# Kernel tuning notes

Hardware: AMD Instinct MI355X
Metric: run time of the kernel (lower is better)

The kernel has to match this reference:

```python
import jax, jax.numpy as jnp
import numpy as np

DN = ('NCHW', 'OIHW', 'NCHW')

def conv3x3(x, w):
    # stride-1, SAME padding, no bias (matches build_conv_layer(..., 3, stride=1, padding='same', bias=False))
    return jax.lax.conv_general_dilated(x, w, window_strides=(1, 1), padding='SAME', dimension_numbers=DN)

def setup_inputs() -> dict:
    key = jax.random.key(0)
    k1, k2, k3, k4 = jax.random.split(key, 4)
    B, C, H, W = 4, 256, 64, 64
    inputs = jax.random.normal(k1, (B, C, H, W), dtype=jnp.float32)
    ref = jax.random.normal(k2, (B, C, H, W), dtype=jnp.float32)
    # xavier-uniform-ish conv weights, [O, I, kH, kW]
    fan = C * 9
    lim = np.sqrt(6.0 / (fan + fan)).astype(np.float32)
    w1 = jax.random.uniform(k3, (C, C, 3, 3), dtype=jnp.float32, minval=-lim, maxval=lim)
    w2 = jax.random.uniform(k4, (C, C, 3, 3), dtype=jnp.float32, minval=-lim, maxval=lim)
    gamma = jnp.float32(0.5)
    return {'inputs': inputs, 'ref': ref, 'w1': w1, 'w2': w2, 'gamma': gamma}

def reference(inputs, ref, w1, w2, gamma):
    # Faithful to source: x0 = relu(conv1(inputs)) is computed then immediately
    # overwritten by a view of x1 (a bug in the original), so inputs only
    # contributes its shape. We execute the dead conv for FLOP parity.
    _dead = jax.nn.relu(conv3x3(inputs, w1))
    x1 = jax.nn.relu(conv3x3(ref, w1))            # [B, C, H, W]
    B, C, H, W = x1.shape
    q = x1.transpose(0, 2, 3, 1).reshape(B, H * W, C)   # [B, HW, C]
    k = x1.reshape(B, C, H * W)                          # [B, C, HW]
    scores = jnp.einsum('bnc,bcm->bnm', q, k)            # [B, HW, HW]
    corr = jax.nn.softmax(scores, axis=1)                # softmax over dim=1 (atypical axis)
    v = jax.nn.relu(conv3x3(ref, w2)).reshape(B, C, H * W)  # [B, C, HW]
    A = jnp.einsum('bcn,bnm->bcm', v, corr).reshape(inputs.shape)
    return A * gamma + ref
```

## Files before the change

kernel.cpp:

```cpp
#include <hip/hip_runtime.h>
#include <math.h>

#define CDIM 256
#define NSEQ 4096
#define HWDIM 64
#define PPIX 4356

typedef unsigned short u16;
typedef __attribute__((ext_vector_type(8))) short bf16x8;
typedef __attribute__((ext_vector_type(4))) float f32x4;
typedef __attribute__((ext_vector_type(16))) float f32x16;

__device__ __forceinline__ u16 f2bf(float f) {
    unsigned u = __float_as_uint(f);
    unsigned r = (u + 0x7FFFu + ((u >> 16) & 1u)) >> 16;
    return (u16)r;
}

__device__ __forceinline__ void gload_lds16(const u16* g, u16* l) {
    __builtin_amdgcn_global_load_lds(
        (const __attribute__((address_space(1))) unsigned int*)g,
        (__attribute__((address_space(3))) unsigned int*)l, 16, 0, 0);
}

__global__ __launch_bounds__(256)
void pad_transpose_kernel(const float* __restrict__ x, u16* __restrict__ padded)
{
    __shared__ float lds[64 * 65];
    const int tid = threadIdx.x;
    const int y = blockIdx.x, c0 = blockIdx.y << 6, b = blockIdx.z;
    #pragma unroll
    for (int i = 0; i < 16; ++i) {
        int f = tid + (i << 8);
        int c = f >> 6, xx = f & 63;
        lds[c * 65 + xx] = x[(((size_t)(b * CDIM + c0 + c)) * HWDIM + y) * HWDIM + xx];
    }
    __syncthreads();
    #pragma unroll
    for (int i = 0; i < 2; ++i) {
        int f = tid + (i << 8);
        int xx = f >> 3, c8 = f & 7;
        union { u16 h[8]; float4 v; } pk;
        #pragma unroll
        for (int j = 0; j < 8; ++j) pk.h[j] = f2bf(lds[(c8 * 8 + j) * 65 + xx]);
        *(float4*)&padded[((size_t)b * PPIX + (y + 1) * 66 + (xx + 1)) * CDIM + c0 + (c8 << 3)] = pk.v;
    }
}

__global__ __launch_bounds__(256)
void w_prepack_kernel(const float* __restrict__ w, u16* __restrict__ wk)
{
    int t = (blockIdx.x << 8) + threadIdx.x;
    const float* wp = w + (size_t)t * 9;
    #pragma unroll
    for (int j = 0; j < 9; ++j) wk[j * 65536 + t] = f2bf(wp[j]);
}

__device__ __forceinline__ void conv_stage(const u16* __restrict__ padded,
                                           const u16* __restrict__ wk,
                                           u16* Xb, u16* Wb,
                                           int b, int y0, int cb, int t,
                                           int wv, int lane)
{
    const int kyx = t >> 2, cib = (t & 3) << 6;
    const int ky = kyx / 3, kx = kyx - ky * 3;
    #pragma unroll
    for (int i = 0; i < 2; ++i) {
        int f = ((i << 2) + wv) << 6;
        int fl = f + lane;
        int r = fl >> 3;
        int gsw = (fl & 7) ^ (r & 7);
        gload_lds16(&padded[((size_t)b * PPIX + (y0 + ky) * 66 + r + kx) * CDIM + cib + (gsw << 3)],
                    Xb + (f << 3));
    }
    #pragma unroll
    for (int i = 0; i < 4; ++i) {
        int f = ((i << 2) + wv) << 6;
        int fl = f + lane;
        int r = fl >> 3;
        int gsw = (fl & 7) ^ (r & 7);
        gload_lds16(&wk[((size_t)kyx << 16) + (size_t)(cb + r) * 256 + cib + (gsw << 3)],
                    Wb + (f << 3));
    }
}

template <bool OA>
__global__ __launch_bounds__(256)
void conv_mfma_kernel(const u16* __restrict__ padded, const u16* __restrict__ wk,
                      u16* __restrict__ out)
{
    __shared__ alignas(16) u16 smem[24576];

    const int tid = threadIdx.x;
    const int lane = tid & 63, wv = tid >> 6;
    const int lr = lane & 15, lg = lane >> 4;
    const int cb = blockIdx.x << 7;
    const int y0 = blockIdx.y;
    const int b = blockIdx.z;

    constexpr int MF = OA ? 4 : 2;
    constexpr int NF = OA ? 2 : 4;
    f32x4 acc[MF][NF] = {};

    conv_stage(padded, wk, smem, smem + 8192, b, y0, cb, 0, wv, lane);
    __syncthreads();

    int cur = 0;
    for (int t = 0; t < 36; ++t) {
        if (t + 1 < 36)
            conv_stage(padded, wk, smem + (cur ^ 1) * 4096,
                       smem + 8192 + (cur ^ 1) * 8192, b, y0, cb, t + 1, wv, lane);

        const u16* Xs = smem + cur * 4096;
        const u16* Ws = smem + 8192 + cur * 8192;

        #pragma unroll
        for (int kk = 0; kk < 2; ++kk) {
            const int ca = ((kk << 5) + (lg << 3)) ^ ((lr & 7) << 3);
            if constexpr (OA) {
                bf16x8 a[4], bb[2];
                #pragma unroll
                for (int mf = 0; mf < 4; ++mf)
                    a[mf] = *(const bf16x8*)&Xs[((mf * 16 + lr) << 6) + ca];
                #pragma unroll
                for (int nf = 0; nf < 2; ++nf)
                    bb[nf] = *(const bf16x8*)&Ws[((wv * 32 + nf * 16 + lr) << 6) + ca];
                #pragma unroll
                for (int mf = 0; mf < 4; ++mf)
                    #pragma unroll
                    for (int nf = 0; nf < 2; ++nf)
                        acc[mf][nf] = __builtin_amdgcn_mfma_f32_16x16x32_bf16(a[mf], bb[nf], acc[mf][nf], 0, 0, 0);
            } else {
                bf16x8 a[2], bb[4];
                #pragma unroll
                for (int mf = 0; mf < 2; ++mf)
                    a[mf] = *(const bf16x8*)&Ws[((wv * 32 + mf * 16 + lr) << 6) + ca];
                #pragma unroll
                for (int nf = 0; nf < 4; ++nf)
                    bb[nf] = *(const bf16x8*)&Xs[((nf * 16 + lr) << 6) + ca];
                #pragma unroll
                for (int mf = 0; mf < 2; ++mf)
                    #pragma unroll
                    for (int nf = 0; nf < 4; ++nf)
                        acc[mf][nf] = __builtin_amdgcn_mfma_f32_16x16x32_bf16(a[mf], bb[nf], acc[mf][nf], 0, 0, 0);
            }
        }
        __syncthreads();
        cur ^= 1;
    }

    const int m0 = y0 << 6;
    if constexpr (OA) {
        #pragma unroll
        for (int mf = 0; mf < 4; ++mf)
            #pragma unroll
            for (int nf = 0; nf < 2; ++nf) {
                int nb = m0 + mf * 16 + lg * 4;
                int co = cb + wv * 32 + nf * 16 + lr;
                union { u16 h[4]; uint2 v; } pk;
                #pragma unroll
                for (int j = 0; j < 4; ++j) pk.h[j] = f2bf(fmaxf(acc[mf][nf][j], 0.f));
                *(uint2*)&out[((size_t)(b * CDIM + co)) * NSEQ + nb] = pk.v;
            }
    } else {
        #pragma unroll
        for (int mf = 0; mf < 2; ++mf)
            #pragma unroll
            for (int nf = 0; nf < 4; ++nf) {
                int cob = cb + wv * 32 + mf * 16 + lg * 4;
                int n = m0 + nf * 16 + lr;
                union { u16 h[4]; uint2 v; } pk;
                #pragma unroll
                for (int j = 0; j < 4; ++j) pk.h[j] = f2bf(fmaxf(acc[mf][nf][j], 0.f));
                *(uint2*)&out[((size_t)(b * NSEQ + n)) * CDIM + cob] = pk.v;
            }
    }
}

__global__ __launch_bounds__(256)
void rownorm_kernel(const u16* __restrict__ XT, float* __restrict__ rn2,
                    float* __restrict__ bmax)
{
    __shared__ float wmax[4];
    const int tid = threadIdx.x;
    const int lane = tid & 63, wv = tid >> 6;
    const int row = (blockIdx.x << 2) + wv;
    const u16* xp = &XT[(size_t)row * CDIM + (lane << 2)];
    uint2 v = *(const uint2*)xp;
    float s = 0.f;
    #pragma unroll
    for (int j = 0; j < 4; ++j) {
        unsigned hu = (j & 1) ? ((&v.x)[j >> 1] >> 16) : ((&v.x)[j >> 1] & 0xFFFFu);
        float x = __uint_as_float(hu << 16);
        s += x * x;
    }
    #pragma unroll
    for (int off = 1; off < 64; off <<= 1) s += __shfl_xor(s, off);
    if (lane == 0) {
        rn2[row] = s;
        wmax[wv] = s;
    }
    __syncthreads();
    if (tid == 0)
        bmax[blockIdx.x] = fmaxf(fmaxf(wmax[0], wmax[1]), fmaxf(wmax[2], wmax[3]));
}

__global__ __launch_bounds__(256)
void maxred_kernel(const float* __restrict__ bmax, float* __restrict__ maxrn2)
{
    __shared__ float wred[4];
    const int tid = threadIdx.x;
    const int lane = tid & 63, wv = tid >> 6;
    const int b = blockIdx.x;
    float m = 0.f;
    #pragma unroll
    for (int i = 0; i < 4; ++i)
        m = fmaxf(m, bmax[(b << 10) + (i << 8) + tid]);
    #pragma unroll
    for (int off = 1; off < 64; off <<= 1) m = fmaxf(m, __shfl_xor(m, off));
    if (lane == 0) wred[wv] = m;
    __syncthreads();
    if (tid == 0)
        maxrn2[b] = fmaxf(fmaxf(wred[0], wred[1]), fmaxf(wred[2], wred[3]));
}

#define M_TILE 128
#define NC 64
#define NCHUNKS 32

#define KS_OFF 0
#define VS_OFF 32768
#define P_OFF  65536

__device__ __forceinline__ void stage_chunk(const u16* __restrict__ XT, const u16* __restrict__ Vn,
                                            u16* Kb, u16* Vb, int b, int n0, int wv, int lane)
{
    #pragma unroll
    for (int i = 0; i < 4; ++i) {
        int f = ((i << 3) + wv) << 6;
        int fl = f + lane;
        int r = fl >> 5;
        int gsw = (fl & 31) ^ (r & 15);
        gload_lds16(&XT[(size_t)(b * NSEQ + n0 + r) * CDIM + (gsw << 3)], Kb + (f << 3));
    }
    #pragma unroll
    for (int i = 0; i < 4; ++i) {
        int f = ((i << 3) + wv) << 6;
        int fl = f + lane;
        int r = fl >> 3;
        int gsw = (fl & 7) ^ (r & 7);
        gload_lds16(&Vn[(size_t)(b * CDIM + r) * NSEQ + n0 + (gsw << 3)], Vb + (f << 3));
    }
}

__global__ __launch_bounds__(512, 2)
void attn_part_kernel(const u16* __restrict__ XT, const u16* __restrict__ Vn,
                      const float* __restrict__ rn2, const float* __restrict__ maxrn2,
                      float* __restrict__ o0, u16* __restrict__ o1,
                      float* __restrict__ lsum)
{
    __shared__ alignas(16) u16 smem[73728];
    u16* Ps = smem + P_OFF;

    const int tid = threadIdx.x;
    const int lane = tid & 63;
    const int wv = tid >> 6;
    const int l31 = lane & 31;
    const int hi = lane >> 5;
    const int bh = blockIdx.x;
    const int b = bh >> 1, h = bh & 1;
    const int m0 = blockIdx.y * M_TILE;
    const int nbase = h * (NSEQ / 2);

    const int qt = wv & 3;
    const int kh = wv >> 2;
    const int qa = qt * 32 + l31;
    const int qsel = wv & 1;
    const int csel = wv >> 1;

    const float mq = sqrtf(rn2[(size_t)b * NSEQ + m0 + qa]) * sqrtf(maxrn2[b]);

    bf16x8 qreg[16];
    {
        const u16* qrow = &XT[(size_t)(b * NSEQ + m0 + qa) * CDIM + (hi << 3)];
        #pragma unroll
        for (int ks = 0; ks < 16; ++ks)
            qreg[ks] = *(const bf16x8*)(qrow + (ks << 4));
    }

    f32x16 o[2][2] = {};
    float lrun = 0.f;

    stage_chunk(XT, Vn, smem + KS_OFF, smem + VS_OFF, b, nbase, wv, lane);
    __syncthreads();

    int cur = 0;
    for (int ci = 0; ci < NCHUNKS; ++ci) {
        if (ci + 1 < NCHUNKS)
            stage_chunk(XT, Vn, smem + KS_OFF + (cur ^ 1) * 16384,
                        smem + VS_OFF + (cur ^ 1) * 16384,
                        b, nbase + (ci + 1) * NC, wv, lane);

        const u16* Kc = smem + KS_OFF + cur * 16384;
        const u16* Vc = smem + VS_OFF + cur * 16384;

        f32x16 s0 = {}, s1 = {};
        {
            const int krow = kh * 32 + l31;
            const u16* kbase = &Kc[krow << 8];
            const int ksw = krow & 15;
            __builtin_amdgcn_s_setprio(1);
            #pragma unroll
            for (int ks = 0; ks < 16; ks += 2) {
                bf16x8 ka0 = *(const bf16x8*)&kbase[((((ks + 0) << 1) + hi) ^ ksw) << 3];
                bf16x8 ka1 = *(const bf16x8*)&kbase[((((ks + 1) << 1) + hi) ^ ksw) << 3];
                s0 = __builtin_amdgcn_mfma_f32_32x32x16_bf16(ka0, qreg[ks], s0, 0, 0, 0);
                s1 = __builtin_amdgcn_mfma_f32_32x32x16_bf16(ka1, qreg[ks + 1], s1, 0, 0, 0);
            }
            __builtin_amdgcn_s_setprio(0);
        }
        f32x16 s = s0 + s1;

        float p[16];
        float ps = 0.f;
        #pragma unroll
        for (int r = 0; r < 16; ++r) { p[r] = __expf(s[r] - mq); ps += p[r]; }
        ps += __shfl_xor(ps, 32);
        lrun += ps;

        {
            const int swz = qa & 7;
            #pragma unroll
            for (int r4 = 0; r4 < 4; ++r4) {
                union { u16 h4[4]; uint2 v; } pk;
                pk.h4[0] = f2bf(p[r4 * 4 + 0]); pk.h4[1] = f2bf(p[r4 * 4 + 1]);
                pk.h4[2] = f2bf(p[r4 * 4 + 2]); pk.h4[3] = f2bf(p[r4 * 4 + 3]);
                int g = (kh << 2) + r4;
                *(uint2*)&Ps[(qa << 6) + (((g ^ swz) << 3) | (hi << 2))] = pk.v;
            }
        }
        __syncthreads();

        {
            const int q0 = ((qsel << 1) + 0) * 32 + l31;
            const int q1 = ((qsel << 1) + 1) * 32 + l31;
            const int c0 = ((csel << 1) + 0) * 32 + l31;
            const int c1 = ((csel << 1) + 1) * 32 + l31;
            __builtin_amdgcn_s_setprio(1);
            #pragma unroll
            for (int ks = 0; ks < 4; ++ks) {
                const int gp = (ks << 1) + hi;
                bf16x8 pb0 = *(const bf16x8*)&Ps[(q0 << 6) + ((gp ^ (q0 & 7)) << 3)];
                bf16x8 pb1 = *(const bf16x8*)&Ps[(q1 << 6) + ((gp ^ (q1 & 7)) << 3)];
                bf16x8 va0 = *(const bf16x8*)&Vc[(c0 << 6) + ((gp ^ (c0 & 7)) << 3)];
                bf16x8 va1 = *(const bf16x8*)&Vc[(c1 << 6) + ((gp ^ (c1 & 7)) << 3)];
                o[0][0] = __builtin_amdgcn_mfma_f32_32x32x16_bf16(va0, pb0, o[0][0], 0, 0, 0);
                o[0][1] = __builtin_amdgcn_mfma_f32_32x32x16_bf16(va1, pb0, o[0][1], 0, 0, 0);
                o[1][0] = __builtin_amdgcn_mfma_f32_32x32x16_bf16(va0, pb1, o[1][0], 0, 0, 0);
                o[1][1] = __builtin_amdgcn_mfma_f32_32x32x16_bf16(va1, pb1, o[1][1], 0, 0, 0);
            }
            __builtin_amdgcn_s_setprio(0);
        }

        __syncthreads();
        cur ^= 1;
    }

    if (lane < 32)
        lsum[(size_t)(((h * 2 + kh) * 4 + b)) * NSEQ + m0 + qa] = lrun;

    #pragma unroll
    for (int qi = 0; qi < 2; ++qi) {
        const int q = m0 + ((qsel << 1) + qi) * 32 + l31;
        #pragma unroll
        for (int cj = 0; cj < 2; ++cj) {
            #pragma unroll
            for (int reg = 0; reg < 16; ++reg) {
                int c = ((csel << 1) + cj) * 32 + (reg & 3) + ((reg >> 2) << 3) + (hi << 2);
                size_t oi = ((size_t)(b * CDIM + c)) * NSEQ + q;
                if (h == 0) o0[oi] = o[qi][cj][reg];
                else        o1[oi] = f2bf(o[qi][cj][reg]);
            }
        }
    }
}

__global__ __launch_bounds__(256)
void merge_kernel(float* __restrict__ out, const u16* __restrict__ o1,
                  const float* __restrict__ lsum, const float* __restrict__ ref,
                  const float* __restrict__ gptr)
{
    const int f = (blockIdx.x << 8) + threadIdx.x;
    const int n4 = f & 1023;
    const int c = (f >> 10) & 255;
    const int b = f >> 18;
    const float g = gptr[0];

    float4 p0 = ((const float4*)out)[f];
    uint2 q1 = *(const uint2*)&o1[((size_t)(b * CDIM + c)) * NSEQ + (n4 << 2)];
    float4 rf = ((const float4*)ref)[f];

    float res[4];
    #pragma unroll
    for (int j = 0; j < 4; ++j) {
        int row = (n4 << 2) + j;
        float l = lsum[(size_t)(0 * 4 + b) * NSEQ + row]
                + lsum[(size_t)(1 * 4 + b) * NSEQ + row]
                + lsum[(size_t)(2 * 4 + b) * NSEQ + row]
                + lsum[(size_t)(3 * 4 + b) * NSEQ + row];
        float rl = 1.0f / l;
        float v0 = ((const float*)&p0)[j];
        unsigned hu = ((j & 1) ? ((&q1.x)[j >> 1] >> 16) : ((&q1.x)[j >> 1] & 0xFFFFu));
        float v1 = __uint_as_float(hu << 16);
        float a = (v0 + v1) * rl;
        res[j] = g * a + ((const float*)&rf)[j];
    }
    ((float4*)out)[f] = *(float4*)res;
}

extern "C" void kernel_launch(void* const* d_in, const int* in_sizes, int n_in,
                              void* d_out, int out_size, void* d_ws, size_t ws_size,
                              hipStream_t stream)
{
    const float* ref = (const float*)d_in[1];
    const float* w1  = (const float*)d_in[2];
    const float* w2  = (const float*)d_in[3];
    const float* gma = (const float*)d_in[4];
    float* out = (float*)d_out;

    u16* XT     = (u16*)d_ws;
    u16* Vn     = XT + (size_t)4 * NSEQ * CDIM;
    u16* padded = Vn + (size_t)4 * NSEQ * CDIM;
    u16* wk1    = padded + (size_t)4 * PPIX * CDIM;
    u16* wk2    = wk1 + (size_t)9 * 65536;
    u16*   o1     = padded;
    float* lsum   = (float*)wk1;
    float* rn2    = (float*)wk2;
    float* bmax   = rn2 + 16384;
    float* maxrn2 = bmax + 4096;

    hipMemsetAsync(padded, 0, (size_t)4 * PPIX * CDIM * sizeof(u16), stream);
    pad_transpose_kernel<<<dim3(64, 4, 4), 256, 0, stream>>>(ref, padded);
    w_prepack_kernel<<<dim3(256), 256, 0, stream>>>(w1, wk1);
    w_prepack_kernel<<<dim3(256), 256, 0, stream>>>(w2, wk2);

    dim3 cgrid(2, 64, 4);
    conv_mfma_kernel<false><<<cgrid, 256, 0, stream>>>(padded, wk1, XT);
    conv_mfma_kernel<true ><<<cgrid, 256, 0, stream>>>(padded, wk2, Vn);

    rownorm_kernel<<<dim3(4096), 256, 0, stream>>>(XT, rn2, bmax);
    maxred_kernel<<<dim3(4), 256, 0, stream>>>(bmax, maxrn2);

    attn_part_kernel<<<dim3(8, NSEQ / M_TILE), 512, 0, stream>>>(XT, Vn, rn2, maxrn2, out, o1, lsum);
    merge_kernel<<<dim3((4 * CDIM * NSEQ / 4) / 256), 256, 0, stream>>>(out, o1, lsum, ref, gma);
}
```

Before: 168.8 us.

## Use 16-wave blocks with 128-key chunks and single-buffered LDS in attention

The attention kernel now runs 1024 threads (16 waves) per block and stages 128 keys per chunk instead of 64, halving the chunk count. The double-buffered K/V staging is replaced by a single buffer with an explicit vmcnt wait and barrier. Each wave now owns one 32-channel slice of the PV product, and the softmax row sums are split into 8 partials that the merge kernel adds up. The goal is fewer barriers per key and more waves to hide latency. The risks are that load/compute overlap is lost without double buffering, and the larger block caps registers per thread, which could cause spills given the 64 registers held for Q.

```diff
diff --git a/kernel.cpp b/kernel.cpp
--- a/kernel.cpp
+++ b/kernel.cpp
@@ -225,19 +225,20 @@
 }
 
 #define M_TILE 128
-#define NC 64
-#define NCHUNKS 32
-
-#define KS_OFF 0
+#define NC 128
+#define NCHUNKS 16
+
 #define VS_OFF 32768
 #define P_OFF  65536
 
-__device__ __forceinline__ void stage_chunk(const u16* __restrict__ XT, const u16* __restrict__ Vn,
-                                            u16* Kb, u16* Vb, int b, int n0, int wv, int lane)
+__device__ __forceinline__ void stage_chunk128(const u16* __restrict__ XT,
+                                               const u16* __restrict__ Vn,
+                                               u16* Kb, u16* Vb,
+                                               int b, int n0, int wid, int lane)
 {
     #pragma unroll
     for (int i = 0; i < 4; ++i) {
-        int f = ((i << 3) + wv) << 6;
+        int f = ((i << 4) + wid) << 6;
         int fl = f + lane;
         int r = fl >> 5;
         int gsw = (fl & 31) ^ (r & 15);
@@ -245,26 +246,26 @@
     }
     #pragma unroll
     for (int i = 0; i < 4; ++i) {
-        int f = ((i << 3) + wv) << 6;
+        int f = ((i << 4) + wid) << 6;
         int fl = f + lane;
-        int r = fl >> 3;
-        int gsw = (fl & 7) ^ (r & 7);
+        int r = fl >> 4;
+        int gsw = (fl & 15) ^ (r & 7);
         gload_lds16(&Vn[(size_t)(b * CDIM + r) * NSEQ + n0 + (gsw << 3)], Vb + (f << 3));
     }
 }
 
-__global__ __launch_bounds__(512, 2)
+__global__ __launch_bounds__(1024, 4)
 void attn_part_kernel(const u16* __restrict__ XT, const u16* __restrict__ Vn,
                       const float* __restrict__ rn2, const float* __restrict__ maxrn2,
                       float* __restrict__ o0, u16* __restrict__ o1,
                       float* __restrict__ lsum)
 {
-    __shared__ alignas(16) u16 smem[73728];
+    __shared__ alignas(16) u16 smem[81920];
     u16* Ps = smem + P_OFF;
 
     const int tid = threadIdx.x;
     const int lane = tid & 63;
-    const int wv = tid >> 6;
+    const int wid = tid >> 6;
     const int l31 = lane & 31;
     const int hi = lane >> 5;
     const int bh = blockIdx.x;
@@ -272,11 +273,11 @@
     const int m0 = blockIdx.y * M_TILE;
     const int nbase = h * (NSEQ / 2);
 
-    const int qt = wv & 3;
-    const int kh = wv >> 2;
+    const int qt = wid & 3;
+    const int kh = wid >> 2;
     const int qa = qt * 32 + l31;
-    const int qsel = wv & 1;
-    const int csel = wv >> 1;
+    const int ct = wid >> 1;
+    const int qp = wid & 1;
 
     const float mq = sqrtf(rn2[(size_t)b * NSEQ + m0 + qa]) * sqrtf(maxrn2[b]);
 
@@ -288,38 +289,28 @@
             qreg[ks] = *(const bf16x8*)(qrow + (ks << 4));
     }
 
-    f32x16 o[2][2] = {};
+    f32x16 o[2] = {};
     float lrun = 0.f;
 
-    stage_chunk(XT, Vn, smem + KS_OFF, smem + VS_OFF, b, nbase, wv, lane);
-    __syncthreads();
-
-    int cur = 0;
     for (int ci = 0; ci < NCHUNKS; ++ci) {
-        if (ci + 1 < NCHUNKS)
-            stage_chunk(XT, Vn, smem + KS_OFF + (cur ^ 1) * 16384,
-                        smem + VS_OFF + (cur ^ 1) * 16384,
-                        b, nbase + (ci + 1) * NC, wv, lane);
-
-        const u16* Kc = smem + KS_OFF + cur * 16384;
-        const u16* Vc = smem + VS_OFF + cur * 16384;
-
-        f32x16 s0 = {}, s1 = {};
+        stage_chunk128(XT, Vn, smem, smem + VS_OFF, b, nbase + ci * NC, wid, lane);
+        asm volatile("s_waitcnt vmcnt(4)" ::: "memory");
+        __builtin_amdgcn_s_barrier();
+        __builtin_amdgcn_sched_barrier(0);
+
+        f32x16 s = {};
         {
             const int krow = kh * 32 + l31;
-            const u16* kbase = &Kc[krow << 8];
+            const u16* kbase = &smem[krow << 8];
             const int ksw = krow & 15;
             __builtin_amdgcn_s_setprio(1);
             #pragma unroll
-            for (int ks = 0; ks < 16; ks += 2) {
-                bf16x8 ka0 = *(const bf16x8*)&kbase[((((ks + 0) << 1) + hi) ^ ksw) << 3];
-                bf16x8 ka1 = *(const bf16x8*)&kbase[((((ks + 1) << 1) + hi) ^ ksw) << 3];
-                s0 = __builtin_amdgcn_mfma_f32_32x32x16_bf16(ka0, qreg[ks], s0, 0, 0, 0);
-                s1 = __builtin_amdgcn_mfma_f32_32x32x16_bf16(ka1, qreg[ks + 1], s1, 0, 0, 0);
+            for (int ks = 0; ks < 16; ++ks) {
+                bf16x8 ka = *(const bf16x8*)&kbase[(((ks << 1) + hi) ^ ksw) << 3];
+                s = __builtin_amdgcn_mfma_f32_32x32x16_bf16(ka, qreg[ks], s, 0, 0, 0);
             }
             __builtin_amdgcn_s_setprio(0);
         }
-        f32x16 s = s0 + s1;
 
         float p[16];
         float ps = 0.f;
@@ -336,51 +327,45 @@
                 pk.h4[0] = f2bf(p[r4 * 4 + 0]); pk.h4[1] = f2bf(p[r4 * 4 + 1]);
                 pk.h4[2] = f2bf(p[r4 * 4 + 2]); pk.h4[3] = f2bf(p[r4 * 4 + 3]);
                 int g = (kh << 2) + r4;
-                *(uint2*)&Ps[(qa << 6) + (((g ^ swz) << 3) | (hi << 2))] = pk.v;
+                *(uint2*)&Ps[(qa << 7) + (((g ^ swz) << 3) | (hi << 2))] = pk.v;
             }
         }
         __syncthreads();
 
         {
-            const int q0 = ((qsel << 1) + 0) * 32 + l31;
-            const int q1 = ((qsel << 1) + 1) * 32 + l31;
-            const int c0 = ((csel << 1) + 0) * 32 + l31;
-            const int c1 = ((csel << 1) + 1) * 32 + l31;
+            const int crow = ct * 32 + l31;
+            const u16* vbase = &smem[VS_OFF + (crow << 7)];
+            const int csw = crow & 7;
+            const int q0 = (qp * 2 + 0) * 32 + l31;
+            const int q1 = (qp * 2 + 1) * 32 + l31;
             __builtin_amdgcn_s_setprio(1);
             #pragma unroll
-            for (int ks = 0; ks < 4; ++ks) {
+            for (int ks = 0; ks < 8; ++ks) {
                 const int gp = (ks << 1) + hi;
-                bf16x8 pb0 = *(const bf16x8*)&Ps[(q0 << 6) + ((gp ^ (q0 & 7)) << 3)];
-                bf16x8 pb1 = *(const bf16x8*)&Ps[(q1 << 6) + ((gp ^ (q1 & 7)) << 3)];
-                bf16x8 va0 = *(const bf16x8*)&Vc[(c0 << 6) + ((gp ^ (c0 & 7)) << 3)];
-                bf16x8 va1 = *(const bf16x8*)&Vc[(c1 << 6) + ((gp ^ (c1 & 7)) << 3)];
-                o[0][0] = __builtin_amdgcn_mfma_f32_32x32x16_bf16(va0, pb0, o[0][0], 0, 0, 0);
-                o[0][1] = __builtin_amdgcn_mfma_f32_32x32x16_bf16(va1, pb0, o[0][1], 0, 0, 0);
-                o[1][0] = __builtin_amdgcn_mfma_f32_32x32x16_bf16(va0, pb1, o[1][0], 0, 0, 0);
-                o[1][1] = __builtin_amdgcn_mfma_f32_32x32x16_bf16(va1, pb1, o[1][1], 0, 0, 0);
+                bf16x8 va  = *(const bf16x8*)&vbase[((gp ^ csw) << 3)];
+                bf16x8 pb0 = *(const bf16x8*)&Ps[(q0 << 7) + ((gp ^ (q0 & 7)) << 3)];
+                bf16x8 pb1 = *(const bf16x8*)&Ps[(q1 << 7) + ((gp ^ (q1 & 7)) << 3)];
+                o[0] = __builtin_amdgcn_mfma_f32_32x32x16_bf16(va, pb0, o[0], 0, 0, 0);
+                o[1] = __builtin_amdgcn_mfma_f32_32x32x16_bf16(va, pb1, o[1], 0, 0, 0);
             }
             __builtin_amdgcn_s_setprio(0);
         }
 
         __syncthreads();
-        cur ^= 1;
     }
 
     if (lane < 32)
-        lsum[(size_t)(((h * 2 + kh) * 4 + b)) * NSEQ + m0 + qa] = lrun;
+        lsum[(size_t)((h * 4 + kh) * 4 + b) * NSEQ + m0 + qa] = lrun;
 
     #pragma unroll
     for (int qi = 0; qi < 2; ++qi) {
-        const int q = m0 + ((qsel << 1) + qi) * 32 + l31;
-        #pragma unroll
-        for (int cj = 0; cj < 2; ++cj) {
-            #pragma unroll
-            for (int reg = 0; reg < 16; ++reg) {
-                int c = ((csel << 1) + cj) * 32 + (reg & 3) + ((reg >> 2) << 3) + (hi << 2);
-                size_t oi = ((size_t)(b * CDIM + c)) * NSEQ + q;
-                if (h == 0) o0[oi] = o[qi][cj][reg];
-                else        o1[oi] = f2bf(o[qi][cj][reg]);
-            }
+        const int q = m0 + (qp * 2 + qi) * 32 + l31;
+        #pragma unroll
+        for (int reg = 0; reg < 16; ++reg) {
+            int c = ct * 32 + (reg & 3) + ((reg >> 2) << 3) + (hi << 2);
+            size_t oi = ((size_t)(b * CDIM + c)) * NSEQ + q;
+            if (h == 0) o0[oi] = o[qi][reg];
+            else        o1[oi] = f2bf(o[qi][reg]);
         }
     }
 }
@@ -404,10 +389,10 @@
     #pragma unroll
     for (int j = 0; j < 4; ++j) {
         int row = (n4 << 2) + j;
-        float l = lsum[(size_t)(0 * 4 + b) * NSEQ + row]
-                + lsum[(size_t)(1 * 4 + b) * NSEQ + row]
-                + lsum[(size_t)(2 * 4 + b) * NSEQ + row]
-                + lsum[(size_t)(3 * 4 + b) * NSEQ + row];
+        float l = 0.f;
+        #pragma unroll
+        for (int sidx = 0; sidx < 8; ++sidx)
+            l += lsum[(size_t)(sidx * 4 + b) * NSEQ + row];
         float rl = 1.0f / l;
         float v0 = ((const float*)&p0)[j];
         unsigned hu = ((j & 1) ? ((&q1.x)[j >> 1] >> 16) : ((&q1.x)[j >> 1] & 0xFFFFu));
@@ -451,6 +436,6 @@
     rownorm_kernel<<<dim3(4096), 256, 0, stream>>>(XT, rn2, bmax);
     maxred_kernel<<<dim3(4), 256, 0, stream>>>(bmax, maxrn2);
 
-    attn_part_kernel<<<dim3(8, NSEQ / M_TILE), 512, 0, stream>>>(XT, Vn, rn2, maxrn2, out, o1, lsum);
+    attn_part_kernel<<<dim3(8, NSEQ / M_TILE), 1024, 0, stream>>>(XT, Vn, rn2, maxrn2, out, o1, lsum);
     merge_kernel<<<dim3((4 * CDIM * NSEQ / 4) / 256), 256, 0, stream>>>(out, o1, lsum, ref, gma);
 }
```

After: 285.8 us. 69.3% more time.

## Fuse both convolutions into one dual-output kernel sharing input tiles

Applied to the files above, without the earlier changes.

Merges the two weight-prepack launches into one kernel, and merges the two conv kernels into a single kernel. Each input tile is staged into LDS once and multiplied against both weight sets, so the padded input is read half as often and launches drop. In the attention kernel, the split dual-accumulator score loop and the s_setprio hints are also removed. The fused conv uses more LDS and twice the accumulator registers, which may lower occupancy. Its grid of 512 blocks carries double work per block, so there is less parallelism than the two separate launches had.

```diff
diff --git a/kernel.cpp b/kernel.cpp
--- a/kernel.cpp
+++ b/kernel.cpp
@@ -48,19 +48,26 @@
 }
 
 __global__ __launch_bounds__(256)
-void w_prepack_kernel(const float* __restrict__ w, u16* __restrict__ wk)
-{
-    int t = (blockIdx.x << 8) + threadIdx.x;
-    const float* wp = w + (size_t)t * 9;
+void w_prepack2_kernel(const float* __restrict__ w1, const float* __restrict__ w2,
+                       u16* __restrict__ wk1, u16* __restrict__ wk2)
+{
+    int g = (blockIdx.x << 8) + threadIdx.x;
+    int t = g & 65535;
+    const float* wp = (g < 65536 ? w1 : w2) + (size_t)t * 9;
+    u16* wk = (g < 65536 ? wk1 : wk2);
     #pragma unroll
     for (int j = 0; j < 9; ++j) wk[j * 65536 + t] = f2bf(wp[j]);
 }
 
-__device__ __forceinline__ void conv_stage(const u16* __restrict__ padded,
-                                           const u16* __restrict__ wk,
-                                           u16* Xb, u16* Wb,
-                                           int b, int y0, int cb, int t,
-                                           int wv, int lane)
+#define CW1_OFF 8192
+#define CW2_OFF 24576
+
+__device__ __forceinline__ void conv_stage2(const u16* __restrict__ padded,
+                                            const u16* __restrict__ wk1,
+                                            const u16* __restrict__ wk2,
+                                            u16* Xb, u16* W1b, u16* W2b,
+                                            int b, int y0, int cb, int t,
+                                            int wv, int lane)
 {
     const int kyx = t >> 2, cib = (t & 3) << 6;
     const int ky = kyx / 3, kx = kyx - ky * 3;
@@ -79,17 +86,26 @@
         int fl = f + lane;
         int r = fl >> 3;
         int gsw = (fl & 7) ^ (r & 7);
-        gload_lds16(&wk[((size_t)kyx << 16) + (size_t)(cb + r) * 256 + cib + (gsw << 3)],
-                    Wb + (f << 3));
-    }
-}
-
-template <bool OA>
-__global__ __launch_bounds__(256)
-void conv_mfma_kernel(const u16* __restrict__ padded, const u16* __restrict__ wk,
-                      u16* __restrict__ out)
-{
-    __shared__ alignas(16) u16 smem[24576];
+        gload_lds16(&wk1[((size_t)kyx << 16) + (size_t)(cb + r) * 256 + cib + (gsw << 3)],
+                    W1b + (f << 3));
+    }
+    #pragma unroll
+    for (int i = 0; i < 4; ++i) {
+        int f = ((i << 2) + wv) << 6;
+        int fl = f + lane;
+        int r = fl >> 3;
+        int gsw = (fl & 7) ^ (r & 7);
+        gload_lds16(&wk2[((size_t)kyx << 16) + (size_t)(cb + r) * 256 + cib + (gsw << 3)],
+                    W2b + (f << 3));
+    }
+}
+
+__global__ __launch_bounds__(256)
+void conv_dual_kernel(const u16* __restrict__ padded,
+                      const u16* __restrict__ wk1, const u16* __restrict__ wk2,
+                      u16* __restrict__ XT, u16* __restrict__ Vn)
+{
+    __shared__ alignas(16) u16 smem[40960];
 
     const int tid = threadIdx.x;
     const int lane = tid & 63, wv = tid >> 6;
@@ -98,83 +114,76 @@
     const int y0 = blockIdx.y;
     const int b = blockIdx.z;
 
-    constexpr int MF = OA ? 4 : 2;
-    constexpr int NF = OA ? 2 : 4;
-    f32x4 acc[MF][NF] = {};
-
-    conv_stage(padded, wk, smem, smem + 8192, b, y0, cb, 0, wv, lane);
+    f32x4 acc1[2][4] = {};
+    f32x4 acc2[4][2] = {};
+
+    conv_stage2(padded, wk1, wk2, smem, smem + CW1_OFF, smem + CW2_OFF,
+                b, y0, cb, 0, wv, lane);
     __syncthreads();
 
     int cur = 0;
     for (int t = 0; t < 36; ++t) {
         if (t + 1 < 36)
-            conv_stage(padded, wk, smem + (cur ^ 1) * 4096,
-                       smem + 8192 + (cur ^ 1) * 8192, b, y0, cb, t + 1, wv, lane);
-
-        const u16* Xs = smem + cur * 4096;
-        const u16* Ws = smem + 8192 + cur * 8192;
+            conv_stage2(padded, wk1, wk2, smem + (cur ^ 1) * 4096,
+                        smem + CW1_OFF + (cur ^ 1) * 8192,
+                        smem + CW2_OFF + (cur ^ 1) * 8192,
+                        b, y0, cb, t + 1, wv, lane);
+
+        const u16* Xs  = smem + cur * 4096;
+        const u16* Ws1 = smem + CW1_OFF + cur * 8192;
+        const u16* Ws2 = smem + CW2_OFF + cur * 8192;
 
         #pragma unroll
         for (int kk = 0; kk < 2; ++kk) {
             const int ca = ((kk << 5) + (lg << 3)) ^ ((lr & 7) << 3);
-            if constexpr (OA) {
-                bf16x8 a[4], bb[2];
+            bf16x8 xs[4];
+            #pragma unroll
+            for (int nf = 0; nf < 4; ++nf)
+                xs[nf] = *(const bf16x8*)&Xs[((nf * 16 + lr) << 6) + ca];
+            bf16x8 w1f[2], w2f[2];
+            #pragma unroll
+            for (int mf = 0; mf < 2; ++mf) {
+                w1f[mf] = *(const bf16x8*)&Ws1[((wv * 32 + mf * 16 + lr) << 6) + ca];
+                w2f[mf] = *(const bf16x8*)&Ws2[((wv * 32 + mf * 16 + lr) << 6) + ca];
+            }
+            #pragma unroll
+            for (int mf = 0; mf < 2; ++mf)
                 #pragma unroll
-                for (int mf = 0; mf < 4; ++mf)
-                    a[mf] = *(const bf16x8*)&Xs[((mf * 16 + lr) << 6) + ca];
+                for (int nf = 0; nf < 4; ++nf)
+                    acc1[mf][nf] = __builtin_amdgcn_mfma_f32_16x16x32_bf16(w1f[mf], xs[nf], acc1[mf][nf], 0, 0, 0);
+            #pragma unroll
+            for (int mf = 0; mf < 4; ++mf)
                 #pragma unroll
                 for (int nf = 0; nf < 2; ++nf)
-                    bb[nf] = *(const bf16x8*)&Ws[((wv * 32 + nf * 16 + lr) << 6) + ca];
-                #pragma unroll
-                for (int mf = 0; mf < 4; ++mf)
-                    #pragma unroll
-                    for (int nf = 0; nf < 2; ++nf)
-                        acc[mf][nf] = __builtin_amdgcn_mfma_f32_16x16x32_bf16(a[mf], bb[nf], acc[mf][nf], 0, 0, 0);
-            } else {
-                bf16x8 a[2], bb[4];
-                #pragma unroll
-                for (int mf = 0; mf < 2; ++mf)
-                    a[mf] = *(const bf16x8*)&Ws[((wv * 32 + mf * 16 + lr) << 6) + ca];
-                #pragma unroll
-                for (int nf = 0; nf < 4; ++nf)
-                    bb[nf] = *(const bf16x8*)&Xs[((nf * 16 + lr) << 6) + ca];
-                #pragma unroll
-                for (int mf = 0; mf < 2; ++mf)
-                    #pragma unroll
-                    for (int nf = 0; nf < 4; ++nf)
-                        acc[mf][nf] = __builtin_amdgcn_mfma_f32_16x16x32_bf16(a[mf], bb[nf], acc[mf][nf], 0, 0, 0);
-            }
+                    acc2[mf][nf] = __builtin_amdgcn_mfma_f32_16x16x32_bf16(xs[mf], w2f[nf], acc2[mf][nf], 0, 0, 0);
         }
         __syncthreads();
         cur ^= 1;
     }
 
     const int m0 = y0 << 6;
-    if constexpr (OA) {
-        #pragma unroll
-        for (int mf = 0; mf < 4; ++mf)
-            #pragma unroll
-            for (int nf = 0; nf < 2; ++nf) {
-                int nb = m0 + mf * 16 + lg * 4;
-                int co = cb + wv * 32 + nf * 16 + lr;
-                union { u16 h[4]; uint2 v; } pk;
-                #pragma unroll
-                for (int j = 0; j < 4; ++j) pk.h[j] = f2bf(fmaxf(acc[mf][nf][j], 0.f));
-                *(uint2*)&out[((size_t)(b * CDIM + co)) * NSEQ + nb] = pk.v;
-            }
-    } else {
-        #pragma unroll
-        for (int mf = 0; mf < 2; ++mf)
-            #pragma unroll
-            for (int nf = 0; nf < 4; ++nf) {
-                int cob = cb + wv * 32 + mf * 16 + lg * 4;
-                int n = m0 + nf * 16 + lr;
-                union { u16 h[4]; uint2 v; } pk;
-                #pragma unroll
-                for (int j = 0; j < 4; ++j) pk.h[j] = f2bf(fmaxf(acc[mf][nf][j], 0.f));
-                *(uint2*)&out[((size_t)(b * NSEQ + n)) * CDIM + cob] = pk.v;
-            }
-    }
+    #pragma unroll
+    for (int mf = 0; mf < 2; ++mf)
+        #pragma unroll
+        for (int nf = 0; nf < 4; ++nf) {
+            int cob = cb + wv * 32 + mf * 16 + lg * 4;
+            int n = m0 + nf * 16 + lr;
+            union { u16 h[4]; uint2 v; } pk;
+            #pragma unroll
+            for (int j = 0; j < 4; ++j) pk.h[j] = f2bf(fmaxf(acc1[mf][nf][j], 0.f));
+            *(uint2*)&XT[((size_t)(b * NSEQ + n)) * CDIM + cob] = pk.v;
+        }
+    #pragma unroll
+    for (int mf = 0; mf < 4; ++mf)
+        #pragma unroll
+        for (int nf = 0; nf < 2; ++nf) {
+            int nb = m0 + mf * 16 + lg * 4;
+            int co = cb + wv * 32 + nf * 16 + lr;
+            union { u16 h[4]; uint2 v; } pk;
+            #pragma unroll
+            for (int j = 0; j < 4; ++j) pk.h[j] = f2bf(fmaxf(acc2[mf][nf][j], 0.f));
+            *(uint2*)&Vn[((size_t)(b * CDIM + co)) * NSEQ + nb] = pk.v;
+        }
 }
 
 __global__ __launch_bounds__(256)
@@ -304,22 +313,17 @@
         const u16* Kc = smem + KS_OFF + cur * 16384;
         const u16* Vc = smem + VS_OFF + cur * 16384;
 
-        f32x16 s0 = {}, s1 = {};
+        f32x16 s = {};
         {
             const int krow = kh * 32 + l31;
             const u16* kbase = &Kc[krow << 8];
             const int ksw = krow & 15;
-            __builtin_amdgcn_s_setprio(1);
-            #pragma unroll
-            for (int ks = 0; ks < 16; ks += 2) {
-                bf16x8 ka0 = *(const bf16x8*)&kbase[((((ks + 0) << 1) + hi) ^ ksw) << 3];
-                bf16x8 ka1 = *(const bf16x8*)&kbase[((((ks + 1) << 1) + hi) ^ ksw) << 3];
-                s0 = __builtin_amdgcn_mfma_f32_32x32x16_bf16(ka0, qreg[ks], s0, 0, 0, 0);
-                s1 = __builtin_amdgcn_mfma_f32_32x32x16_bf16(ka1, qreg[ks + 1], s1, 0, 0, 0);
+            #pragma unroll
+            for (int ks = 0; ks < 16; ++ks) {
+                bf16x8 ka = *(const bf16x8*)&kbase[(((ks << 1) + hi) ^ ksw) << 3];
+                s = __builtin_amdgcn_mfma_f32_32x32x16_bf16(ka, qreg[ks], s, 0, 0, 0);
             }
-            __builtin_amdgcn_s_setprio(0);
-        }
-        f32x16 s = s0 + s1;
+        }
 
         float p[16];
         float ps = 0.f;
@@ -346,7 +350,6 @@
             const int q1 = ((qsel << 1) + 1) * 32 + l31;
             const int c0 = ((csel << 1) + 0) * 32 + l31;
             const int c1 = ((csel << 1) + 1) * 32 + l31;
-            __builtin_amdgcn_s_setprio(1);
             #pragma unroll
             for (int ks = 0; ks < 4; ++ks) {
                 const int gp = (ks << 1) + hi;
@@ -359,7 +362,6 @@
                 o[1][0] = __builtin_amdgcn_mfma_f32_32x32x16_bf16(va0, pb1, o[1][0], 0, 0, 0);
                 o[1][1] = __builtin_amdgcn_mfma_f32_32x32x16_bf16(va1, pb1, o[1][1], 0, 0, 0);
             }
-            __builtin_amdgcn_s_setprio(0);
         }
 
         __syncthreads();
@@ -441,12 +443,9 @@
 
     hipMemsetAsync(padded, 0, (size_t)4 * PPIX * CDIM * sizeof(u16), stream);
     pad_transpose_kernel<<<dim3(64, 4, 4), 256, 0, stream>>>(ref, padded);
-    w_prepack_kernel<<<dim3(256), 256, 0, stream>>>(w1, wk1);
-    w_prepack_kernel<<<dim3(256), 256, 0, stream>>>(w2, wk2);
-
-    dim3 cgrid(2, 64, 4);
-    conv_mfma_kernel<false><<<cgrid, 256, 0, stream>>>(padded, wk1, XT);
-    conv_mfma_kernel<true ><<<cgrid, 256, 0, stream>>>(padded, wk2, Vn);
+    w_prepack2_kernel<<<dim3(512), 256, 0, stream>>>(w1, w2, wk1, wk2);
+
+    conv_dual_kernel<<<dim3(2, 64, 4), 256, 0, stream>>>(padded, wk1, wk2, XT, Vn);
 
     rownorm_kernel<<<dim3(4096), 256, 0, stream>>>(XT, rn2, bmax);
     maxred_kernel<<<dim3(4), 256, 0, stream>>>(bmax, maxrn2);
```

Result: faster. 159.0 us (-5.8%).
